# Performance work log

Hardware: AMD Instinct MI355X
Metric: run time of the kernel (lower is better)

## Reference

```python
import jax, jax.numpy as jnp
import numpy as np

B, T, C, H = 128, 512, 128, 64  # batch, seq, n_embd, head_size


def setup_inputs() -> dict:
    key = jax.random.key(0)
    ks = jax.random.split(key, 6)
    s = 1.0 / np.sqrt(C)
    return {
        "x": jax.random.normal(ks[0], (B, T, C), dtype=jnp.float32),
        "Wg": jax.random.normal(ks[1], (C, C), dtype=jnp.float32) * s,
        "bg": jnp.zeros((C,), dtype=jnp.float32),
        "Wk": jax.random.normal(ks[2], (C, H), dtype=jnp.float32) * s,
        "Wq": jax.random.normal(ks[3], (C, H), dtype=jnp.float32) * s,
        "Wv": jax.random.normal(ks[4], (C, H), dtype=jnp.float32) * s,
    }


def reference(x, Wg, bg, Wk, Wq, Wv):
    # GateLayer: x * sigmoid(Linear(x))
    g = jax.nn.sigmoid(jnp.einsum('btc,cd->btd', x, Wg) + bg)
    xg = x * g
    k = jnp.einsum('btc,ch->bth', xg, Wk)
    q = jnp.einsum('btc,ch->bth', xg, Wq)
    v = jnp.einsum('btc,ch->bth', xg, Wv)
    # NOTE: original scales by C**-0.5 (n_embd), not head_size**-0.5
    scale = C ** -0.5
    wei = jnp.einsum('bqh,bkh->bqk', q, k) * scale  # [B,T,T]
    causal = jnp.tril(jnp.ones((T, T), dtype=bool))
    wei = jnp.where(causal, wei, -jnp.inf)
    wei = jax.nn.softmax(wei, axis=-1)
    # dropout is identity in eval mode
    out = jnp.einsum('bqk,bkh->bqh', wei, v)  # [B,T,H]
    return out
```

## Files before the change

kernel.cpp:

```cpp
#include <hip/hip_runtime.h>


#define BB 128
#define TB 512
#define CC 128
#define HH 64

static constexpr float SCALE = 0.088388347648318447f;

typedef __attribute__((ext_vector_type(8))) short bf16x8;
typedef __attribute__((ext_vector_type(8))) unsigned short u16x8;
typedef __attribute__((ext_vector_type(4))) float f32x4;

__device__ inline unsigned short f2bf(float f) {
    union { float f; unsigned u; } x; x.f = f;
    unsigned r = x.u + 0x7fff + ((x.u >> 16) & 1);
    return (unsigned short)(r >> 16);
}
__device__ inline float bf2f(unsigned short h) {
    union { unsigned u; float f; } x; x.u = ((unsigned)h) << 16;
    return x.f;
}
__device__ inline bf16x8 pack8(float4 a, float4 b) {
    bf16x8 o;
    o[0] = (short)f2bf(a.x); o[1] = (short)f2bf(a.y);
    o[2] = (short)f2bf(a.z); o[3] = (short)f2bf(a.w);
    o[4] = (short)f2bf(b.x); o[5] = (short)f2bf(b.y);
    o[6] = (short)f2bf(b.z); o[7] = (short)f2bf(b.w);
    return o;
}

__global__ void prep_weights(const float* __restrict__ Wg, const float* __restrict__ Wk,
                             const float* __restrict__ Wq, const float* __restrict__ Wv,
                             unsigned short* __restrict__ WgT, unsigned short* __restrict__ WkT,
                             unsigned short* __restrict__ WqT, unsigned short* __restrict__ WvT)
{
    int idx = blockIdx.x * 256 + threadIdx.x;
    if (idx < 16384) {
        int n = idx >> 7, k = idx & 127;
        WgT[idx] = f2bf(Wg[k * CC + n]);
    } else {
        int j = idx - 16384;
        int mtx = j >> 13;
        int r = j & 8191;
        int n = r >> 7, k = r & 127;
        const float* W = (mtx == 0) ? Wk : (mtx == 1) ? Wq : Wv;
        unsigned short* WT = (mtx == 0) ? WkT : (mtx == 1) ? WqT : WvT;
        WT[r] = f2bf(W[k * HH + n]);
    }
}

__global__ __launch_bounds__(256, 2) void gate_qkv_kernel(
    const float* __restrict__ x, const float* __restrict__ bg,
    const unsigned short* __restrict__ WgT, const unsigned short* __restrict__ WkT,
    const unsigned short* __restrict__ WqT, const unsigned short* __restrict__ WvT,
    unsigned short* __restrict__ qo, unsigned short* __restrict__ ko,
    unsigned short* __restrict__ vto)
{
    __shared__ unsigned short xgs[128 * 136];
    __shared__ unsigned short vpark[4 * 64 * 34];

    const int tid  = threadIdx.x;
    const int wv   = tid >> 6;
    const int lane = tid & 63;
    const int l15  = lane & 15;
    const int quad = lane >> 4;
    const int R0   = blockIdx.x * 128;
    const int row0 = R0 + 32 * wv;

    bf16x8 bx[2][4];
#pragma unroll
    for (int mt = 0; mt < 2; ++mt)
#pragma unroll
        for (int kc = 0; kc < 4; ++kc) {
            const float* p = x + (size_t)(row0 + 16 * mt + l15) * CC + kc * 32 + quad * 8;
            float4 a = *(const float4*)p;
            float4 c = *(const float4*)(p + 4);
            bx[mt][kc] = pack8(a, c);
        }

    float4 xe[8][2];
#pragma unroll
    for (int nt = 0; nt < 8; ++nt)
#pragma unroll
        for (int mt = 0; mt < 2; ++mt)
            xe[nt][mt] = *(const float4*)(x + (size_t)(row0 + 16 * mt + l15) * CC +
                                          16 * nt + 4 * quad);

    f32x4 acc[8][2];
#pragma unroll
    for (int nt = 0; nt < 8; ++nt)
#pragma unroll
        for (int mt = 0; mt < 2; ++mt) acc[nt][mt] = (f32x4){0.f, 0.f, 0.f, 0.f};

    bf16x8 awA[4], awB[4];
#pragma unroll
    for (int kc = 0; kc < 4; ++kc)
        awA[kc] = *(const bf16x8*)(WgT + l15 * CC + kc * 32 + quad * 8);

#pragma unroll
    for (int nt = 0; nt < 8; ++nt) {
        if (nt < 7) {
#pragma unroll
            for (int kc = 0; kc < 4; ++kc)
                awB[kc] = *(const bf16x8*)(WgT + (16 * (nt + 1) + l15) * CC + kc * 32 + quad * 8);
        } else {
#pragma unroll
            for (int kc = 0; kc < 4; ++kc)
                awB[kc] = *(const bf16x8*)(WkT + l15 * CC + kc * 32 + quad * 8);
        }
#pragma unroll
        for (int mt = 0; mt < 2; ++mt)
#pragma unroll
            for (int kc = 0; kc < 4; ++kc)
                acc[nt][mt] = __builtin_amdgcn_mfma_f32_16x16x32_bf16(
                    awA[kc], bx[mt][kc], acc[nt][mt], 0, 0, 0);
#pragma unroll
        for (int kc = 0; kc < 4; ++kc) awA[kc] = awB[kc];
    }

#pragma unroll
    for (int nt = 0; nt < 8; ++nt) {
        float4 bgv = *(const float4*)(bg + 16 * nt + 4 * quad);
#pragma unroll
        for (int mt = 0; mt < 2; ++mt) {
            int m = 32 * wv + 16 * mt + l15;
            float e0 = __expf(-(acc[nt][mt][0] + bgv.x));
            float e1 = __expf(-(acc[nt][mt][1] + bgv.y));
            float e2 = __expf(-(acc[nt][mt][2] + bgv.z));
            float e3 = __expf(-(acc[nt][mt][3] + bgv.w));
            ushort4 o;
            o.x = f2bf(xe[nt][mt].x * __builtin_amdgcn_rcpf(1.f + e0));
            o.y = f2bf(xe[nt][mt].y * __builtin_amdgcn_rcpf(1.f + e1));
            o.z = f2bf(xe[nt][mt].z * __builtin_amdgcn_rcpf(1.f + e2));
            o.w = f2bf(xe[nt][mt].w * __builtin_amdgcn_rcpf(1.f + e3));
            *(ushort4*)(xgs + m * 136 + 16 * nt + 4 * quad) = o;
        }
    }

    bf16x8 bxg[2][4];
#pragma unroll
    for (int mt = 0; mt < 2; ++mt)
#pragma unroll
        for (int kc = 0; kc < 4; ++kc)
            bxg[mt][kc] = *(const bf16x8*)(xgs + (32 * wv + 16 * mt + l15) * 136 +
                                           kc * 32 + quad * 8);

    const int b = R0 >> 9, t0 = R0 & 511;
    unsigned short* vp = vpark + wv * (64 * 34);
#pragma unroll
    for (int pj = 0; pj < 3; ++pj) {
        f32x4 pacc[4][2];
#pragma unroll
        for (int nt = 0; nt < 4; ++nt)
#pragma unroll
            for (int mt = 0; mt < 2; ++mt) pacc[nt][mt] = (f32x4){0.f, 0.f, 0.f, 0.f};

#pragma unroll
        for (int nt = 0; nt < 4; ++nt) {
            if (!(pj == 2 && nt == 3)) {
                const unsigned short* Wcur = (pj == 0) ? WkT : (pj == 1) ? WqT : WvT;
                const unsigned short* Wnxt = (pj == 0) ? WqT : WvT;
                const unsigned short* Wp   = (nt < 3) ? Wcur : Wnxt;
                const int ntn = (nt < 3) ? nt + 1 : 0;
#pragma unroll
                for (int kc = 0; kc < 4; ++kc)
                    awB[kc] = *(const bf16x8*)(Wp + (16 * ntn + l15) * CC + kc * 32 + quad * 8);
            }
#pragma unroll
            for (int mt = 0; mt < 2; ++mt)
#pragma unroll
                for (int kc = 0; kc < 4; ++kc)
                    pacc[nt][mt] = __builtin_amdgcn_mfma_f32_16x16x32_bf16(
                        awA[kc], bxg[mt][kc], pacc[nt][mt], 0, 0, 0);
#pragma unroll
            for (int kc = 0; kc < 4; ++kc) awA[kc] = awB[kc];
        }

        if (pj < 2) {
            unsigned short* O = (pj == 0) ? ko : qo;
#pragma unroll
            for (int nt = 0; nt < 4; ++nt)
#pragma unroll
                for (int mt = 0; mt < 2; ++mt) {
                    int m = 32 * wv + 16 * mt + l15;
                    ushort4 h;
                    h.x = f2bf(pacc[nt][mt][0]); h.y = f2bf(pacc[nt][mt][1]);
                    h.z = f2bf(pacc[nt][mt][2]); h.w = f2bf(pacc[nt][mt][3]);
                    *(ushort4*)(O + (size_t)(R0 + m) * HH + 16 * nt + quad * 4) = h;
                }
        } else {
#pragma unroll
            for (int nt = 0; nt < 4; ++nt)
#pragma unroll
                for (int mt = 0; mt < 2; ++mt) {
                    int tloc = 16 * mt + l15;
#pragma unroll
                    for (int r = 0; r < 4; ++r)
                        vp[(16 * nt + 4 * quad + r) * 34 + tloc] = f2bf(pacc[nt][mt][r]);
                }
            unsigned short* dst = vto + (size_t)b * (HH * TB) + (size_t)lane * TB +
                                  t0 + 32 * wv;
#pragma unroll
            for (int c = 0; c < 4; ++c) {
                u16x8 vv = *(const u16x8*)(vp + lane * 34 + 8 * c);
                *(u16x8*)(dst + 8 * c) = vv;
            }
        }
    }
}

__device__ __forceinline__ void pv_nomax(const f32x4* s, f32x4& lacc, f32x4* o4,
                                         unsigned short* ps, const bf16x8* bv0,
                                         const bf16x8* bv1, const bf16x8 ones,
                                         int wave, int l15, int quad)
{
#pragma unroll
    for (int nt = 0; nt < 4; ++nt)
#pragma unroll
        for (int r = 0; r < 4; ++r)
            ps[(16 * wave + quad * 4 + r) * 76 + 16 * nt + l15] = f2bf(__expf(s[nt][r]));

    bf16x8 ap0 = *(const bf16x8*)(ps + (16 * wave + l15) * 76 + quad * 8);
    bf16x8 ap1 = *(const bf16x8*)(ps + (16 * wave + l15) * 76 + 32 + quad * 8);
    lacc = __builtin_amdgcn_mfma_f32_16x16x32_bf16(ap0, ones, lacc, 0, 0, 0);
    lacc = __builtin_amdgcn_mfma_f32_16x16x32_bf16(ap1, ones, lacc, 0, 0, 0);
#pragma unroll
    for (int nt = 0; nt < 4; ++nt) {
        o4[nt] = __builtin_amdgcn_mfma_f32_16x16x32_bf16(ap0, bv0[nt], o4[nt], 0, 0, 0);
        o4[nt] = __builtin_amdgcn_mfma_f32_16x16x32_bf16(ap1, bv1[nt], o4[nt], 0, 0, 0);
    }
}

__device__ __forceinline__ void attn_epilogue(const f32x4* o4, const f32x4 lacc,
                                              float* out, size_t base, int q0,
                                              int wave, int l15, int quad)
{
    float inv[4];
#pragma unroll
    for (int r = 0; r < 4; ++r) inv[r] = __builtin_amdgcn_rcpf(lacc[r]);
#pragma unroll
    for (int nt = 0; nt < 4; ++nt)
#pragma unroll
        for (int r = 0; r < 4; ++r)
            out[base + (size_t)(q0 + 16 * wave + quad * 4 + r) * HH + 16 * nt + l15] =
                o4[nt][r] * inv[r];
}

__global__ __launch_bounds__(256, 2) void attn_kernel(
    const unsigned short* __restrict__ q, const unsigned short* __restrict__ k,
    const unsigned short* __restrict__ vt, float* __restrict__ out)
{
    __shared__ unsigned short ks[64 * 72];
    __shared__ unsigned short vs[64 * 72];
    __shared__ unsigned short ps[64 * 76];

    const int tid  = threadIdx.x;
    const int wave = tid >> 6;
    const int lane = tid & 63;
    const int l15  = lane & 15;
    const int quad = lane >> 4;
    const int pr   = blockIdx.x;
    const int b    = blockIdx.y;
    const size_t base = (size_t)b * TB * HH;

    const int qtA = pr, qtB = 7 - pr;
    const int q0A = qtA * 64, q0B = qtB * 64;

    bf16x8 ones;
#pragma unroll
    for (int i = 0; i < 8; ++i) ones[i] = (short)0x3F80;

    const int r0 = tid >> 3, c8 = (tid & 7) * 8;
    const int r1 = r0 + 32;

    bf16x8 kr0 = *(const bf16x8*)(k + base + (size_t)r0 * HH + c8);
    bf16x8 kr1 = *(const bf16x8*)(k + base + (size_t)r1 * HH + c8);
    bf16x8 vr0 = *(const bf16x8*)(vt + base + (size_t)r0 * TB + c8);
    bf16x8 vr1 = *(const bf16x8*)(vt + base + (size_t)r1 * TB + c8);

    const unsigned short* qrA = q + base + (size_t)(q0A + 16 * wave + l15) * HH;
    const unsigned short* qrB = q + base + (size_t)(q0B + 16 * wave + l15) * HH;
    bf16x8 aqA0 = *(const bf16x8*)(qrA + quad * 8);
    bf16x8 aqA1 = *(const bf16x8*)(qrA + 32 + quad * 8);
    bf16x8 aqB0 = *(const bf16x8*)(qrB + quad * 8);
    bf16x8 aqB1 = *(const bf16x8*)(qrB + 32 + quad * 8);

    f32x4 oA[4], oB[4], lAacc, lBacc;
#pragma unroll
    for (int nt = 0; nt < 4; ++nt) {
        oA[nt] = (f32x4){0.f, 0.f, 0.f, 0.f};
        oB[nt] = (f32x4){0.f, 0.f, 0.f, 0.f};
    }
    lAacc = (f32x4){0.f, 0.f, 0.f, 0.f};
    lBacc = (f32x4){0.f, 0.f, 0.f, 0.f};

    const int nIt = qtB + 1;
    for (int kt = 0; kt < nIt; ++kt) {
        __syncthreads();
        *(bf16x8*)(ks + r0 * 72 + c8) = kr0;
        *(bf16x8*)(ks + r1 * 72 + c8) = kr1;
        *(bf16x8*)(vs + r0 * 72 + c8) = vr0;
        *(bf16x8*)(vs + r1 * 72 + c8) = vr1;
        __syncthreads();

        if (kt + 1 < nIt) {
            const int k0n = (kt + 1) * 64;
            kr0 = *(const bf16x8*)(k + base + (size_t)(k0n + r0) * HH + c8);
            kr1 = *(const bf16x8*)(k + base + (size_t)(k0n + r1) * HH + c8);
            vr0 = *(const bf16x8*)(vt + base + (size_t)r0 * TB + k0n + c8);
            vr1 = *(const bf16x8*)(vt + base + (size_t)r1 * TB + k0n + c8);
        }

        bf16x8 bk0[4], bk1[4], bv0[4], bv1[4];
#pragma unroll
        for (int nt = 0; nt < 4; ++nt) {
            bk0[nt] = *(const bf16x8*)(ks + (16 * nt + l15) * 72 + quad * 8);
            bk1[nt] = *(const bf16x8*)(ks + (16 * nt + l15) * 72 + 32 + quad * 8);
            bv0[nt] = *(const bf16x8*)(vs + (16 * nt + l15) * 72 + quad * 8);
            bv1[nt] = *(const bf16x8*)(vs + (16 * nt + l15) * 72 + 32 + quad * 8);
        }

        const bool actA = (kt <= qtA);

        f32x4 sA[4], sB[4];
#pragma unroll
        for (int nt = 0; nt < 4; ++nt) {
            f32x4 zb = (f32x4){0.f, 0.f, 0.f, 0.f};
            zb = __builtin_amdgcn_mfma_f32_16x16x32_bf16(aqB0, bk0[nt], zb, 0, 0, 0);
            zb = __builtin_amdgcn_mfma_f32_16x16x32_bf16(aqB1, bk1[nt], zb, 0, 0, 0);
            sB[nt] = zb;
            if (actA) {
                f32x4 za = (f32x4){0.f, 0.f, 0.f, 0.f};
                za = __builtin_amdgcn_mfma_f32_16x16x32_bf16(aqA0, bk0[nt], za, 0, 0, 0);
                za = __builtin_amdgcn_mfma_f32_16x16x32_bf16(aqA1, bk1[nt], za, 0, 0, 0);
                sA[nt] = za;
            }
        }

        if (actA) {
            const bool diagA = (kt == qtA);
#pragma unroll
            for (int nt = 0; nt < 4; ++nt)
#pragma unroll
                for (int r = 0; r < 4; ++r) {
                    float sv = sA[nt][r] * SCALE;
                    if (diagA && (16 * nt + l15) > (16 * wave + quad * 4 + r)) sv = -1e30f;
                    sA[nt][r] = sv;
                }
            pv_nomax(sA, lAacc, oA, ps, bv0, bv1, ones, wave, l15, quad);
            if (diagA) attn_epilogue(oA, lAacc, out, base, q0A, wave, l15, quad);
        }

        {
            const bool diagB = (kt == qtB);
#pragma unroll
            for (int nt = 0; nt < 4; ++nt)
#pragma unroll
                for (int r = 0; r < 4; ++r) {
                    float sv = sB[nt][r] * SCALE;
                    if (diagB && (16 * nt + l15) > (16 * wave + quad * 4 + r)) sv = -1e30f;
                    sB[nt][r] = sv;
                }
            pv_nomax(sB, lBacc, oB, ps, bv0, bv1, ones, wave, l15, quad);
        }
    }

    attn_epilogue(oB, lBacc, out, base, q0B, wave, l15, quad);
}

extern "C" void kernel_launch(void* const* d_in, const int* in_sizes, int n_in,
                              void* d_out, int out_size, void* d_ws, size_t ws_size,
                              hipStream_t stream) {
    const float* x  = (const float*)d_in[0];
    const float* Wg = (const float*)d_in[1];
    const float* bg = (const float*)d_in[2];
    const float* Wk = (const float*)d_in[3];
    const float* Wq = (const float*)d_in[4];
    const float* Wv = (const float*)d_in[5];
    float* out = (float*)d_out;

    unsigned short* ws = (unsigned short*)d_ws;
    const size_t BTH = (size_t)BB * TB * HH;
    unsigned short* qo  = ws;
    unsigned short* ko  = ws + BTH;
    unsigned short* vto = ws + 2 * BTH;
    unsigned short* WgT = ws + 3 * BTH;
    unsigned short* WkT = WgT + 16384;
    unsigned short* WqT = WkT + 8192;
    unsigned short* WvT = WqT + 8192;

    hipLaunchKernelGGL(prep_weights, dim3(160), dim3(256), 0, stream,
                       Wg, Wk, Wq, Wv, WgT, WkT, WqT, WvT);
    hipLaunchKernelGGL(gate_qkv_kernel, dim3(BB * TB / 128), dim3(256), 0, stream,
                       x, bg, WgT, WkT, WqT, WvT, qo, ko, vto);
    hipLaunchKernelGGL(attn_kernel, dim3(4, BB), dim3(256), 0, stream,
                       qo, ko, vto, out);
}
```

Baseline: 132.1 us.

## Stage gate and QKV weights in LDS, shrink per-wave gated-x buffer

The gate_qkv kernel now cooperatively loads the gate weight matrix into shared memory, and then the K/Q/V weights, instead of having each wave stream them from global memory with register double-buffering. The gated activations go into a small per-wave slice buffer, interleaved with the gate epilogue, rather than a full 128-row tile. The V-transpose staging buffer is removed, and V^T is written directly to global with strided 2-byte stores. This trades redundant global or L2 weight fetches for block barriers and LDS traffic. The uncoalesced V^T stores may cost global-memory efficiency.

```diff
diff --git a/kernel.cpp b/kernel.cpp
--- a/kernel.cpp
+++ b/kernel.cpp
@@ -57,8 +57,8 @@
     unsigned short* __restrict__ qo, unsigned short* __restrict__ ko,
     unsigned short* __restrict__ vto)
 {
-    __shared__ unsigned short xgs[128 * 136];
-    __shared__ unsigned short vpark[4 * 64 * 34];
+    __shared__ unsigned short wlds[192 * 136];
+    __shared__ unsigned short slice[4][32 * 40];
 
     const int tid  = threadIdx.x;
     const int wv   = tid >> 6;
@@ -68,6 +68,13 @@
     const int R0   = blockIdx.x * 128;
     const int row0 = R0 + 32 * wv;
 
+#pragma unroll
+    for (int it = 0; it < 8; ++it) {
+        int idx = tid + 256 * it;
+        int r = idx >> 4, c8 = idx & 15;
+        *(u16x8*)(wlds + r * 136 + c8 * 8) = *(const u16x8*)(WgT + r * 128 + c8 * 8);
+    }
+
     bf16x8 bx[2][4];
 #pragma unroll
     for (int mt = 0; mt < 2; ++mt)
@@ -87,67 +94,67 @@
             xe[nt][mt] = *(const float4*)(x + (size_t)(row0 + 16 * mt + l15) * CC +
                                           16 * nt + 4 * quad);
 
+    __syncthreads();
+
     f32x4 acc[8][2];
 #pragma unroll
     for (int nt = 0; nt < 8; ++nt)
 #pragma unroll
         for (int mt = 0; mt < 2; ++mt) acc[nt][mt] = (f32x4){0.f, 0.f, 0.f, 0.f};
 
-    bf16x8 awA[4], awB[4];
-#pragma unroll
-    for (int kc = 0; kc < 4; ++kc)
-        awA[kc] = *(const bf16x8*)(WgT + l15 * CC + kc * 32 + quad * 8);
-
 #pragma unroll
     for (int nt = 0; nt < 8; ++nt) {
-        if (nt < 7) {
-#pragma unroll
-            for (int kc = 0; kc < 4; ++kc)
-                awB[kc] = *(const bf16x8*)(WgT + (16 * (nt + 1) + l15) * CC + kc * 32 + quad * 8);
-        } else {
-#pragma unroll
-            for (int kc = 0; kc < 4; ++kc)
-                awB[kc] = *(const bf16x8*)(WkT + l15 * CC + kc * 32 + quad * 8);
+#pragma unroll
+        for (int kc = 0; kc < 4; ++kc) {
+            bf16x8 aw = *(const bf16x8*)(wlds + (16 * nt + l15) * 136 + kc * 32 + quad * 8);
+#pragma unroll
+            for (int mt = 0; mt < 2; ++mt)
+                acc[nt][mt] = __builtin_amdgcn_mfma_f32_16x16x32_bf16(
+                    aw, bx[mt][kc], acc[nt][mt], 0, 0, 0);
+        }
+    }
+
+    unsigned short* sl = slice[wv];
+    bf16x8 bxg[2][4];
+#pragma unroll
+    for (int kc = 0; kc < 4; ++kc) {
+#pragma unroll
+        for (int half = 0; half < 2; ++half) {
+            int nt = 2 * kc + half;
+            float4 bgv = *(const float4*)(bg + 16 * nt + 4 * quad);
+#pragma unroll
+            for (int mt = 0; mt < 2; ++mt) {
+                float e0 = __expf(-(acc[nt][mt][0] + bgv.x));
+                float e1 = __expf(-(acc[nt][mt][1] + bgv.y));
+                float e2 = __expf(-(acc[nt][mt][2] + bgv.z));
+                float e3 = __expf(-(acc[nt][mt][3] + bgv.w));
+                ushort4 o;
+                o.x = f2bf(xe[nt][mt].x * __builtin_amdgcn_rcpf(1.f + e0));
+                o.y = f2bf(xe[nt][mt].y * __builtin_amdgcn_rcpf(1.f + e1));
+                o.z = f2bf(xe[nt][mt].z * __builtin_amdgcn_rcpf(1.f + e2));
+                o.w = f2bf(xe[nt][mt].w * __builtin_amdgcn_rcpf(1.f + e3));
+                *(ushort4*)(sl + (16 * mt + l15) * 40 + 16 * half + 4 * quad) = o;
+            }
         }
 #pragma unroll
         for (int mt = 0; mt < 2; ++mt)
-#pragma unroll
-            for (int kc = 0; kc < 4; ++kc)
-                acc[nt][mt] = __builtin_amdgcn_mfma_f32_16x16x32_bf16(
-                    awA[kc], bx[mt][kc], acc[nt][mt], 0, 0, 0);
-#pragma unroll
-        for (int kc = 0; kc < 4; ++kc) awA[kc] = awB[kc];
-    }
-
-#pragma unroll
-    for (int nt = 0; nt < 8; ++nt) {
-        float4 bgv = *(const float4*)(bg + 16 * nt + 4 * quad);
-#pragma unroll
-        for (int mt = 0; mt < 2; ++mt) {
-            int m = 32 * wv + 16 * mt + l15;
-            float e0 = __expf(-(acc[nt][mt][0] + bgv.x));
-            float e1 = __expf(-(acc[nt][mt][1] + bgv.y));
-            float e2 = __expf(-(acc[nt][mt][2] + bgv.z));
-            float e3 = __expf(-(acc[nt][mt][3] + bgv.w));
-            ushort4 o;
-            o.x = f2bf(xe[nt][mt].x * __builtin_amdgcn_rcpf(1.f + e0));
-            o.y = f2bf(xe[nt][mt].y * __builtin_amdgcn_rcpf(1.f + e1));
-            o.z = f2bf(xe[nt][mt].z * __builtin_amdgcn_rcpf(1.f + e2));
-            o.w = f2bf(xe[nt][mt].w * __builtin_amdgcn_rcpf(1.f + e3));
-            *(ushort4*)(xgs + m * 136 + 16 * nt + 4 * quad) = o;
-        }
-    }
-
-    bf16x8 bxg[2][4];
-#pragma unroll
-    for (int mt = 0; mt < 2; ++mt)
-#pragma unroll
-        for (int kc = 0; kc < 4; ++kc)
-            bxg[mt][kc] = *(const bf16x8*)(xgs + (32 * wv + 16 * mt + l15) * 136 +
-                                           kc * 32 + quad * 8);
+            bxg[mt][kc] = *(const bf16x8*)(sl + (16 * mt + l15) * 40 + quad * 8);
+    }
+
+    __syncthreads();
+
+#pragma unroll
+    for (int it = 0; it < 12; ++it) {
+        int idx = tid + 256 * it;
+        int r = idx >> 4, c8 = idx & 15;
+        const unsigned short* src = (r < 64) ? (WkT + r * 128)
+                                  : (r < 128) ? (WqT + (r - 64) * 128)
+                                              : (WvT + (r - 128) * 128);
+        *(u16x8*)(wlds + r * 136 + c8 * 8) = *(const u16x8*)(src + c8 * 8);
+    }
+    __syncthreads();
 
     const int b = R0 >> 9, t0 = R0 & 511;
-    unsigned short* vp = vpark + wv * (64 * 34);
 #pragma unroll
     for (int pj = 0; pj < 3; ++pj) {
         f32x4 pacc[4][2];
@@ -158,23 +165,15 @@
 
 #pragma unroll
         for (int nt = 0; nt < 4; ++nt) {
-            if (!(pj == 2 && nt == 3)) {
-                const unsigned short* Wcur = (pj == 0) ? WkT : (pj == 1) ? WqT : WvT;
-                const unsigned short* Wnxt = (pj == 0) ? WqT : WvT;
-                const unsigned short* Wp   = (nt < 3) ? Wcur : Wnxt;
-                const int ntn = (nt < 3) ? nt + 1 : 0;
-#pragma unroll
-                for (int kc = 0; kc < 4; ++kc)
-                    awB[kc] = *(const bf16x8*)(Wp + (16 * ntn + l15) * CC + kc * 32 + quad * 8);
+#pragma unroll
+            for (int kc = 0; kc < 4; ++kc) {
+                bf16x8 aw = *(const bf16x8*)(wlds + (64 * pj + 16 * nt + l15) * 136 +
+                                             kc * 32 + quad * 8);
+#pragma unroll
+                for (int mt = 0; mt < 2; ++mt)
+                    pacc[nt][mt] = __builtin_amdgcn_mfma_f32_16x16x32_bf16(
+                        aw, bxg[mt][kc], pacc[nt][mt], 0, 0, 0);
             }
-#pragma unroll
-            for (int mt = 0; mt < 2; ++mt)
-#pragma unroll
-                for (int kc = 0; kc < 4; ++kc)
-                    pacc[nt][mt] = __builtin_amdgcn_mfma_f32_16x16x32_bf16(
-                        awA[kc], bxg[mt][kc], pacc[nt][mt], 0, 0, 0);
-#pragma unroll
-            for (int kc = 0; kc < 4; ++kc) awA[kc] = awB[kc];
         }
 
         if (pj < 2) {
@@ -194,18 +193,13 @@
             for (int nt = 0; nt < 4; ++nt)
 #pragma unroll
                 for (int mt = 0; mt < 2; ++mt) {
-                    int tloc = 16 * mt + l15;
+                    int m = 32 * wv + 16 * mt + l15;
+                    unsigned short* dst =
+                        vto + (size_t)b * (HH * TB) + (16 * nt + quad * 4) * TB + t0 + m;
 #pragma unroll
                     for (int r = 0; r < 4; ++r)
-                        vp[(16 * nt + 4 * quad + r) * 34 + tloc] = f2bf(pacc[nt][mt][r]);
+                        dst[r * TB] = f2bf(pacc[nt][mt][r]);
                 }
-            unsigned short* dst = vto + (size_t)b * (HH * TB) + (size_t)lane * TB +
-                                  t0 + 32 * wv;
-#pragma unroll
-            for (int c = 0; c < 4; ++c) {
-                u16x8 vv = *(const u16x8*)(vp + lane * 34 + 8 * c);
-                *(u16x8*)(dst + 8 * c) = vv;
-            }
         }
     }
 }
```

New measurement: 120.0 us. 1.1x faster.
